# Kernel tuning notes

Measured on AMD Instinct MI355X. Metric: run time of the kernel, lower is better.

## Reference

```python
import jax, jax.numpy as jnp
import numpy as np

M = 4  # block size for overlapped mode
NEG = -1e30  # stands in for -inf; exp(NEG - max) == 0 exactly in fp32


def setup_inputs() -> dict:
    key = jax.random.key(0)
    ks = jax.random.split(key, 8)
    B, T, d, c = 4, 8192, 1024, 128
    return {
        "H": jax.random.normal(ks[0], (B, T, d), dtype=jnp.float32),
        "W_a_KV": jax.random.normal(ks[1], (d, c), dtype=jnp.float32),
        "W_b_KV": jax.random.normal(ks[2], (d, c), dtype=jnp.float32),
        "W_a_Z": jax.random.normal(ks[3], (d, c), dtype=jnp.float32),
        "W_b_Z": jax.random.normal(ks[4], (d, c), dtype=jnp.float32),
        "B_a": jax.random.normal(ks[5], (M, c), dtype=jnp.float32),
        "B_b": jax.random.normal(ks[6], (M, c), dtype=jnp.float32),
    }


def reference(H, W_a_KV, W_b_KV, W_a_Z, W_b_Z, B_a, B_b):
    B, T, d = H.shape
    c = W_a_KV.shape[1]
    nb = T // M  # number of blocks

    # dense projections (cuBLAS-equivalent GEMMs)
    C_a = (H @ W_a_KV).reshape(B, nb, M, c)
    C_b = (H @ W_b_KV).reshape(B, nb, M, c)
    Z_a = (H @ W_a_Z).reshape(B, nb, M, c) + B_a  # bias broadcast over blocks
    Z_b = (H @ W_b_Z).reshape(B, nb, M, c) + B_b

    # block i attends to its own block (a) and the PREVIOUS block (b);
    # block 0 has no previous block -> masked logits / zero values
    Z_b_prev = jnp.concatenate(
        [jnp.full((B, 1, M, c), NEG, dtype=H.dtype), Z_b[:, :-1]], axis=1)
    C_b_prev = jnp.concatenate(
        [jnp.zeros((B, 1, M, c), dtype=H.dtype), C_b[:, :-1]], axis=1)

    logits = jnp.concatenate([Z_a, Z_b_prev], axis=2)   # [B, nb, 2M, c]
    vals = jnp.concatenate([C_a, C_b_prev], axis=2)     # [B, nb, 2M, c]
    probs = jax.nn.softmax(logits, axis=2)              # softmax over 2M window
    return (probs * vals).sum(axis=2)                   # [B, nb, c]
```

## Files before the change

### kernel.cpp

```cpp
#include <hip/hip_runtime.h>
#include <hip/hip_fp16.h>

typedef _Float16 f16;
typedef _Float16 f16x8 __attribute__((ext_vector_type(8)));
typedef float f32x16 __attribute__((ext_vector_type(16)));

#define NEGV (-1e30f)

constexpr int T_    = 8192;
constexpr int BATCH = 4;
constexpr int D_    = 1024;
constexpr int C_    = 128;
constexpr int ROWS  = BATCH * T_;
constexpr int BM    = 128;
constexpr int BK    = 64;
constexpr int KT    = D_ / BK;
constexpr int NWG   = ROWS / BM;
constexpr int NTHR  = 512;

#define BOUND_OFF (1u << 20)

__device__ __forceinline__ void gload_lds16(const void* g, void* l) {
  __builtin_amdgcn_global_load_lds(
      (const __attribute__((address_space(1))) void*)g,
      (__attribute__((address_space(3))) void*)l, 16, 0, 0);
}

__global__ __launch_bounds__(1024) void tc_prep(
    const float* __restrict__ H,
    const float* __restrict__ Wakv, const float* __restrict__ Wbkv,
    const float* __restrict__ Waz,  const float* __restrict__ Wbz,
    unsigned char* __restrict__ ws)
{
  const int b = blockIdx.x, t = threadIdx.x;
  if (b < NWG) {
    float* bound = (float*)(ws + BOUND_OFF) + (long long)b * 1024;
    if ((b & 63) == 0) {
      bound[t] = (t < 512) ? 0.f : NEGV;
      return;
    }
    __shared__ float hrow[4][1024];
    __shared__ float part[8][8][128];
    const long long R0 = (long long)b * BM - 4;
    for (int i = t; i < 4096; i += 1024) hrow[i >> 10][i & 1023] = H[R0 * D_ + i];
    __syncthreads();

    const int j  = t & 127;
    const int kc = t >> 7;
    const int k0 = kc * 128;
    float acc[2][4] = {{0.f,0.f,0.f,0.f},{0.f,0.f,0.f,0.f}};
#pragma unroll 4
    for (int k = k0; k < k0 + 128; ++k) {
      const float w0 = Wbkv[k*128 + j];
      const float w1 = Wbz [k*128 + j];
#pragma unroll
      for (int m = 0; m < 4; ++m) {
        const float hv = hrow[m][k];
        acc[0][m] += hv * w0;
        acc[1][m] += hv * w1;
      }
    }
#pragma unroll
    for (int half = 0; half < 2; ++half)
#pragma unroll
      for (int m = 0; m < 4; ++m) part[kc][half*4 + m][j] = acc[half][m];
    __syncthreads();

    {
      const int half = t >> 9, rm = (t >> 7) & 3, jj = t & 127;
      float s = 0.f;
#pragma unroll
      for (int kk = 0; kk < 8; ++kk) s += part[kk][half*4 + rm][jj];
      bound[t] = s;
    }
  } else {
    const int u   = (b - NWG) * 1024 + t;
    const int kt  = u >> 12;
    const int rem = u & 4095;
    const int k8  = rem >> 9;
    const int col = rem & 511;
    const int mat = col >> 7, j = col & 127;
    const float* Wm = (mat == 0) ? Wakv : (mat == 1) ? Wbkv : (mat == 2) ? Waz : Wbz;
    f16x8 v;
#pragma unroll
    for (int e = 0; e < 8; ++e) v[e] = (f16)Wm[(kt*64 + k8*8 + e)*128 + j];
    *(f16x8*)(ws + (size_t)kt*65536 + col*128 + ((k8*16) ^ ((col & 7) << 4))) = v;
  }
}

__global__ __launch_bounds__(NTHR, 2) void tc_main(
    const float* __restrict__ H,
    const float* __restrict__ Ba,
    const float* __restrict__ Bbb,
    const unsigned char* __restrict__ ws,
    float* __restrict__ out)
{
  __shared__ __align__(16) unsigned char lds[16384 + 2*65536];
  unsigned char* sA  = lds;
  unsigned char* sB0 = lds + 16384;
  unsigned char* sB1 = lds + 16384 + 65536;

  const int tid  = threadIdx.x;
  const int w    = tid >> 6;
  const int lane = tid & 63;
  const int g    = blockIdx.x;
  const long long R0 = (long long)g * BM;

  f32x16 acc[2][4];
#pragma unroll
  for (int i = 0; i < 2; ++i)
#pragma unroll
    for (int jq = 0; jq < 4; ++jq)
#pragma unroll
      for (int e = 0; e < 16; ++e) acc[i][jq][e] = 0.f;

  const int ar   = tid >> 2;
  const int akq  = tid & 3;
  const float* aptr = H + (R0 + ar) * D_ + akq * 16;
  const int abase = ar * 128;
  const int aswz  = (ar & 7) << 4;

  const int whalf = w >> 2;
  const int jpos  = w & 3;
  const int mrow  = lane & 31;
  const int kq2   = (lane >> 5) * 16;
  const int axor  = (mrow & 7) << 4;
  const int arow0 = (whalf*64 + mrow) * 128;
  const int arow1 = arow0 + 32*128;
  const int jb    = (jpos*32 + mrow) * 128;

  float4 areg[4];

#pragma unroll
  for (int r = 0; r < 8; ++r)
    gload_lds16(ws + (size_t)0*65536 + w*1024 + r*8192 + lane*16, sB0 + w*1024 + r*8192);
  {
    const float4* p = (const float4*)aptr;
    areg[0] = p[0]; areg[1] = p[1]; areg[2] = p[2]; areg[3] = p[3];
  }

  for (int kt = 0; kt < KT; ++kt) {
    {
      f16x8 v0, v1;
      const float* af = (const float*)areg;
#pragma unroll
      for (int e = 0; e < 8; ++e) { v0[e] = (f16)af[e]; v1[e] = (f16)af[8 + e]; }
      *(f16x8*)(sA + abase + ((akq*32)      ^ aswz)) = v0;
      *(f16x8*)(sA + abase + ((akq*32 + 16) ^ aswz)) = v1;
    }
    const int ktn = (kt + 1) & (KT - 1);
    unsigned char* sBn = ((kt + 1) & 1) ? sB1 : sB0;
#pragma unroll
    for (int r = 0; r < 8; ++r)
      gload_lds16(ws + (size_t)ktn*65536 + w*1024 + r*8192 + lane*16, sBn + w*1024 + r*8192);

    __builtin_amdgcn_sched_barrier(0);
    asm volatile("s_waitcnt vmcnt(8) lgkmcnt(0)" ::: "memory");
    __builtin_amdgcn_sched_barrier(0);
    __builtin_amdgcn_s_barrier();
    __builtin_amdgcn_sched_barrier(0);

    {
      const float4* p = (const float4*)(aptr + ktn * 64);
      areg[0] = p[0]; areg[1] = p[1]; areg[2] = p[2]; areg[3] = p[3];
    }

    const unsigned char* sBc = (kt & 1) ? sB1 : sB0;
#pragma unroll
    for (int kf = 0; kf < 4; ++kf) {
      const int ko = ((kf*32 + kq2) ^ axor);
      f16x8 a0 = *(const f16x8*)(sA + arow0 + ko);
      f16x8 a1 = *(const f16x8*)(sA + arow1 + ko);
#pragma unroll
      for (int gr = 0; gr < 4; ++gr) {
        f16x8 bv = *(const f16x8*)(sBc + gr*16384 + jb + ko);
        acc[0][gr] = __builtin_amdgcn_mfma_f32_32x32x16_f16(a0, bv, acc[0][gr], 0, 0, 0);
        acc[1][gr] = __builtin_amdgcn_mfma_f32_32x32x16_f16(a1, bv, acc[1][gr], 0, 0, 0);
      }
    }

    __builtin_amdgcn_sched_barrier(0);
    __builtin_amdgcn_s_barrier();
    __builtin_amdgcn_sched_barrier(0);
  }

  asm volatile("s_waitcnt vmcnt(0)" ::: "memory");
  __builtin_amdgcn_s_barrier();

  float* eCb = (float*)lds;
  float* eZb = (float*)(lds + 65536);
  const int jj = jpos*32 + mrow;
  const int h  = lane >> 5;

#pragma unroll
  for (int rf = 0; rf < 2; ++rf)
#pragma unroll
    for (int r = 0; r < 16; ++r) {
      const int row = whalf*64 + rf*32 + (r & 3) + 8*(r >> 2) + 4*h;
      eCb[row*128 + jj] = acc[rf][1][r];
      eZb[row*128 + jj] = acc[rf][3][r];
    }
  __syncthreads();

  float bav[4], bbv[4];
#pragma unroll
  for (int m = 0; m < 4; ++m) { bav[m] = Ba[m*128 + jj]; bbv[m] = Bbb[m*128 + jj]; }
  const float* bound = (const float*)(ws + BOUND_OFF) + (long long)g * 1024;

#pragma unroll
  for (int rf = 0; rf < 2; ++rf)
#pragma unroll
    for (int q = 0; q < 4; ++q) {
      const int bf = 2*q + h;
      const int bl = whalf*16 + rf*8 + bf;
      float za[4], ca[4], zb[4], cb[4];
#pragma unroll
      for (int m = 0; m < 4; ++m) {
        za[m] = acc[rf][2][q*4 + m] + bav[m];
        ca[m] = acc[rf][0][q*4 + m];
      }
      if (bl == 0) {
#pragma unroll
        for (int m = 0; m < 4; ++m) {
          cb[m] = bound[m*128 + jj];
          zb[m] = bound[512 + m*128 + jj] + bbv[m];
        }
      } else {
#pragma unroll
        for (int m = 0; m < 4; ++m) {
          const int pr = bl*4 - 4 + m;
          cb[m] = eCb[pr*128 + jj];
          zb[m] = eZb[pr*128 + jj] + bbv[m];
        }
      }
      float mx = za[0];
#pragma unroll
      for (int m = 1; m < 4; ++m) mx = fmaxf(mx, za[m]);
#pragma unroll
      for (int m = 0; m < 4; ++m) mx = fmaxf(mx, zb[m]);
      float s = 0.f, o = 0.f;
#pragma unroll
      for (int m = 0; m < 4; ++m) {
        const float ea = __expf(za[m] - mx);
        const float eb = __expf(zb[m] - mx);
        s += ea + eb;
        o += ea*ca[m] + eb*cb[m];
      }
      out[((long long)g*32 + bl)*128 + jj] = o / s;
    }
}

extern "C" void kernel_launch(void* const* d_in, const int* in_sizes, int n_in,
                              void* d_out, int out_size, void* d_ws, size_t ws_size,
                              hipStream_t stream) {
  const float* H    = (const float*)d_in[0];
  const float* Wakv = (const float*)d_in[1];
  const float* Wbkv = (const float*)d_in[2];
  const float* Waz  = (const float*)d_in[3];
  const float* Wbz  = (const float*)d_in[4];
  const float* Ba   = (const float*)d_in[5];
  const float* Bbb  = (const float*)d_in[6];
  float* out        = (float*)d_out;
  unsigned char* ws = (unsigned char*)d_ws;

  tc_prep<<<NWG + 64, 1024, 0, stream>>>(H, Wakv, Wbkv, Waz, Wbz, ws);
  tc_main<<<NWG, NTHR, 0, stream>>>(H, Ba, Bbb, ws, out);
}
```

Baseline: 65.70 us.

## Double-buffer A tile and split K-step into two ping-pong MFMA phases

Restructures the main GEMM loop so the A tile is double-buffered in LDS alongside B. Each K-step is split into two halves: fragments are read into registers, then MFMAs run at raised priority (s_setprio) while the next stage's global loads and the A conversion/write proceed between barriers. The goal is to overlap LDS reads, global loads and matrix math better than the single-buffered A path did. In exchange it uses more LDS (160KB, which likely allows only one workgroup per CU despite launch_bounds 2), adds more barriers and fragment registers, and waits on vmcnt(0) each iteration.

```diff
diff --git a/kernel.cpp b/kernel.cpp
--- a/kernel.cpp
+++ b/kernel.cpp
@@ -10,7 +10,6 @@
 constexpr int T_    = 8192;
 constexpr int BATCH = 4;
 constexpr int D_    = 1024;
-constexpr int C_    = 128;
 constexpr int ROWS  = BATCH * T_;
 constexpr int BM    = 128;
 constexpr int BK    = 64;
@@ -65,7 +64,6 @@
 #pragma unroll
       for (int m = 0; m < 4; ++m) part[kc][half*4 + m][j] = acc[half][m];
     __syncthreads();
-
     {
       const int half = t >> 9, rm = (t >> 7) & 3, jj = t & 127;
       float s = 0.f;
@@ -95,10 +93,7 @@
     const unsigned char* __restrict__ ws,
     float* __restrict__ out)
 {
-  __shared__ __align__(16) unsigned char lds[16384 + 2*65536];
-  unsigned char* sA  = lds;
-  unsigned char* sB0 = lds + 16384;
-  unsigned char* sB1 = lds + 16384 + 65536;
+  __shared__ __align__(16) unsigned char lds[163840];
 
   const int tid  = threadIdx.x;
   const int w    = tid >> 6;
@@ -130,62 +125,84 @@
   const int jb    = (jpos*32 + mrow) * 128;
 
   float4 areg[4];
-
-#pragma unroll
-  for (int r = 0; r < 8; ++r)
-    gload_lds16(ws + (size_t)0*65536 + w*1024 + r*8192 + lane*16, sB0 + w*1024 + r*8192);
-  {
-    const float4* p = (const float4*)aptr;
-    areg[0] = p[0]; areg[1] = p[1]; areg[2] = p[2]; areg[3] = p[3];
+  f16x8 ra0[2], ra1[2], rb[2][4];
+
+#define SA_OFF(IDX) ((IDX) * 16384)
+#define SB_OFF(IDX) (32768 + (IDX) * 65536)
+
+#define STAGE_B(KTN, DSTOFF)                                                     \
+  { _Pragma("unroll")                                                            \
+    for (int r = 0; r < 8; ++r)                                                  \
+      gload_lds16(ws + (size_t)(KTN)*65536 + w*1024 + r*8192 + lane*16,          \
+                  lds + (DSTOFF) + w*1024 + r*8192); }
+
+#define LOAD_AREG(KTN)                                                           \
+  { const float4* p = (const float4*)(aptr + (KTN) * 64);                        \
+    areg[0] = p[0]; areg[1] = p[1]; areg[2] = p[2]; areg[3] = p[3]; }
+
+#define WRITE_A(DSTOFF)                                                          \
+  { f16x8 v0, v1; const float* af = (const float*)areg;                          \
+    _Pragma("unroll")                                                            \
+    for (int e = 0; e < 8; ++e) { v0[e] = (f16)af[e]; v1[e] = (f16)af[8 + e]; }  \
+    *(f16x8*)(lds + (DSTOFF) + abase + ((akq*32)      ^ aswz)) = v0;             \
+    *(f16x8*)(lds + (DSTOFF) + abase + ((akq*32 + 16) ^ aswz)) = v1; }
+
+#define READ_SUBS(SAOFF, SBOFF, KF0)                                             \
+  { _Pragma("unroll")                                                            \
+    for (int kk = 0; kk < 2; ++kk) {                                             \
+      const int ko = ((((KF0) + kk)*32 + kq2) ^ axor);                           \
+      ra0[kk] = *(const f16x8*)(lds + (SAOFF) + arow0 + ko);                     \
+      ra1[kk] = *(const f16x8*)(lds + (SAOFF) + arow1 + ko);                     \
+      _Pragma("unroll")                                                          \
+      for (int gr = 0; gr < 4; ++gr)                                             \
+        rb[kk][gr] = *(const f16x8*)(lds + (SBOFF) + gr*16384 + jb + ko); } }
+
+#define MFMA_SUBS()                                                              \
+  { _Pragma("unroll")                                                            \
+    for (int kk = 0; kk < 2; ++kk)                                               \
+      _Pragma("unroll")                                                          \
+      for (int gr = 0; gr < 4; ++gr) {                                           \
+        acc[0][gr] = __builtin_amdgcn_mfma_f32_32x32x16_f16(ra0[kk], rb[kk][gr], acc[0][gr], 0, 0, 0); \
+        acc[1][gr] = __builtin_amdgcn_mfma_f32_32x32x16_f16(ra1[kk], rb[kk][gr], acc[1][gr], 0, 0, 0); } }
+
+  LOAD_AREG(0);
+  __builtin_amdgcn_sched_barrier(0);
+  STAGE_B(0, SB_OFF(0));
+  WRITE_A(SA_OFF(0));
+  asm volatile("s_waitcnt vmcnt(0) lgkmcnt(0)" ::: "memory");
+  __builtin_amdgcn_sched_barrier(0);
+  __builtin_amdgcn_s_barrier();
+
+  for (int kt = 0; kt < KT; ++kt) {
+    const int cur = kt & 1, nxt = cur ^ 1;
+    const int ktn = (kt + 1) & (KT - 1);
+    const int saOff = SA_OFF(cur), sbOff = SB_OFF(cur);
+
+    LOAD_AREG(ktn);
+    __builtin_amdgcn_sched_barrier(0);
+    STAGE_B(ktn, SB_OFF(nxt));
+    READ_SUBS(saOff, sbOff, 0);
+    __builtin_amdgcn_s_barrier();
+    asm volatile("s_waitcnt lgkmcnt(0)" ::: "memory");
+    __builtin_amdgcn_sched_barrier(0);
+    __builtin_amdgcn_s_setprio(1);
+    MFMA_SUBS();
+    __builtin_amdgcn_s_setprio(0);
+    __builtin_amdgcn_sched_barrier(0);
+    __builtin_amdgcn_s_barrier();
+
+    READ_SUBS(saOff, sbOff, 2);
+    WRITE_A(SA_OFF(nxt));
+    asm volatile("s_waitcnt vmcnt(0) lgkmcnt(0)" ::: "memory");
+    __builtin_amdgcn_sched_barrier(0);
+    __builtin_amdgcn_s_barrier();
+    __builtin_amdgcn_sched_barrier(0);
+    __builtin_amdgcn_s_setprio(1);
+    MFMA_SUBS();
+    __builtin_amdgcn_s_setprio(0);
+    __builtin_amdgcn_sched_barrier(0);
+    __builtin_amdgcn_s_barrier();
   }
-
-  for (int kt = 0; kt < KT; ++kt) {
-    {
-      f16x8 v0, v1;
-      const float* af = (const float*)areg;
-#pragma unroll
-      for (int e = 0; e < 8; ++e) { v0[e] = (f16)af[e]; v1[e] = (f16)af[8 + e]; }
-      *(f16x8*)(sA + abase + ((akq*32)      ^ aswz)) = v0;
-      *(f16x8*)(sA + abase + ((akq*32 + 16) ^ aswz)) = v1;
-    }
-    const int ktn = (kt + 1) & (KT - 1);
-    unsigned char* sBn = ((kt + 1) & 1) ? sB1 : sB0;
-#pragma unroll
-    for (int r = 0; r < 8; ++r)
-      gload_lds16(ws + (size_t)ktn*65536 + w*1024 + r*8192 + lane*16, sBn + w*1024 + r*8192);
-
-    __builtin_amdgcn_sched_barrier(0);
-    asm volatile("s_waitcnt vmcnt(8) lgkmcnt(0)" ::: "memory");
-    __builtin_amdgcn_sched_barrier(0);
-    __builtin_amdgcn_s_barrier();
-    __builtin_amdgcn_sched_barrier(0);
-
-    {
-      const float4* p = (const float4*)(aptr + ktn * 64);
-      areg[0] = p[0]; areg[1] = p[1]; areg[2] = p[2]; areg[3] = p[3];
-    }
-
-    const unsigned char* sBc = (kt & 1) ? sB1 : sB0;
-#pragma unroll
-    for (int kf = 0; kf < 4; ++kf) {
-      const int ko = ((kf*32 + kq2) ^ axor);
-      f16x8 a0 = *(const f16x8*)(sA + arow0 + ko);
-      f16x8 a1 = *(const f16x8*)(sA + arow1 + ko);
-#pragma unroll
-      for (int gr = 0; gr < 4; ++gr) {
-        f16x8 bv = *(const f16x8*)(sBc + gr*16384 + jb + ko);
-        acc[0][gr] = __builtin_amdgcn_mfma_f32_32x32x16_f16(a0, bv, acc[0][gr], 0, 0, 0);
-        acc[1][gr] = __builtin_amdgcn_mfma_f32_32x32x16_f16(a1, bv, acc[1][gr], 0, 0, 0);
-      }
-    }
-
-    __builtin_amdgcn_sched_barrier(0);
-    __builtin_amdgcn_s_barrier();
-    __builtin_amdgcn_sched_barrier(0);
-  }
-
-  asm volatile("s_waitcnt vmcnt(0)" ::: "memory");
-  __builtin_amdgcn_s_barrier();
 
   float* eCb = (float*)lds;
   float* eZb = (float*)(lds + 65536);
```

Result: slower. 78.16 us (+19.0%).
